# Kernel optimization log

Hardware: AMD Instinct MI355X
Metric: run time of the kernel (lower is better)

Reference implementation:

```python
import jax, jax.numpy as jnp
import numpy as np

B, T, F, H = 4096, 60, 128, 256

def setup_inputs() -> dict:
    key = jax.random.key(0)
    ks = jax.random.split(key, 14)
    sk = 1.0 / np.sqrt(H)
    def unif(k, shape):
        return jax.random.uniform(k, shape, jnp.float32, -sk, sk)
    return {
        "x": jax.random.normal(ks[0], (B, T, F), jnp.float32),
        "Wf": unif(ks[1], (F + H, H)), "bf": unif(ks[2], (H,)),
        "Wu": unif(ks[3], (F + H, H)), "bu": unif(ks[4], (H,)),
        "Wc": unif(ks[5], (F + H, H)), "bc": unif(ks[6], (H,)),
        "Wo": unif(ks[7], (F + H, H)), "bo": unif(ks[8], (H,)),
        "Wd1": jax.random.normal(ks[9], (H, H), jnp.float32) * np.sqrt(2.0 / H),
        "bd1": jnp.zeros((H,), jnp.float32),
        "Wd2": jax.random.normal(ks[10], (H, 1), jnp.float32) * np.sqrt(2.0 / H),
        "bd2": jnp.zeros((1,), jnp.float32),
    }

def reference(x, Wf, bf, Wu, bu, Wc, bc, Wo, bo, Wd1, bd1, Wd2, bd2):
    b = x.shape[0]
    h0 = jnp.zeros((b, H), x.dtype)
    c0 = jnp.zeros((b, H), x.dtype)

    def step(carry, xt):
        h, c = carry
        z = jnp.concatenate([xt, h], axis=-1)  # [B, F+H]
        f = jax.nn.sigmoid(z @ Wf + bf)
        u = jax.nn.sigmoid(z @ Wu + bu)
        g = jnp.tanh(z @ Wc + bc)
        o = jax.nn.sigmoid(z @ Wo + bo)
        c_new = f * c + u * g
        h_new = o * jnp.tanh(c_new)
        return (h_new, c_new), None

    (h, _), _ = jax.lax.scan(step, (h0, c0), jnp.swapaxes(x, 0, 1))  # scan over T
    # dense head: two stacked linear layers, no intermediate activation
    out = (h @ Wd1 + bd1) @ Wd2 + bd2  # [B, 1]
    return out
```

## Files before the change

### kernel.cpp

```cpp
#include <hip/hip_runtime.h>


#define T_STEPS 60
#define F_DIM 128
#define H_DIM 256
#define BC 16
#define ZQ 31.75f
#define L2E 1.44269504f

typedef __attribute__((ext_vector_type(4))) int intx4;

__device__ __forceinline__ int q8(float v) {
    return __float2int_rn(fminf(fmaxf(v, -127.f), 127.f));
}

__global__ __launch_bounds__(1024)
void prep_kernel(const float* __restrict__ Wf, const float* __restrict__ Wu,
                 const float* __restrict__ Wc, const float* __restrict__ Wo,
                 const float* __restrict__ Wd1, const float* __restrict__ bd1,
                 const float* __restrict__ Wd2, const float* __restrict__ bd2,
                 float* __restrict__ cscale, intx4* __restrict__ qpack,
                 float* __restrict__ vhead, float* __restrict__ shead) {
    const int t = threadIdx.x;
    const int b = blockIdx.x;
    if (b < 8) {
        __shared__ float red[16][128];
        __shared__ float fsc[128];
        const int g = b >> 1, ch = b & 1;
        const float* W = (g == 0) ? Wf : (g == 1) ? Wu : (g == 2) ? Wc : Wo;
        const int col = ch * 128 + (t & 127);
        const int grp = t >> 7;
        float mx = 1e-20f, mh = 1e-20f;
#pragma unroll 4
        for (int i = 0; i < 16; ++i)
            mx = fmaxf(mx, fabsf(W[(size_t)(grp * 16 + i) * H_DIM + col]));
#pragma unroll 4
        for (int i = 0; i < 32; ++i)
            mh = fmaxf(mh, fabsf(W[(size_t)(128 + grp * 32 + i) * H_DIM + col]));
        red[grp][t & 127] = mx;
        red[8 + grp][t & 127] = mh;
        __syncthreads();
        if (t < 128) {
            float Mx = red[0][t], Mh = red[8][t];
#pragma unroll
            for (int i = 1; i < 8; ++i) {
                Mx = fmaxf(Mx, red[i][t]);
                Mh = fmaxf(Mh, red[8 + i][t]);
            }
            float cs = fmaxf(4.f * Mx, Mh) * (1.f / 16129.f);
            cscale[g * 256 + ch * 128 + t] = cs;
            fsc[t] = 1.f / (127.f * cs);
        }
        __syncthreads();
#pragma unroll
        for (int i = 0; i < 3; ++i) {
            int task = i * 1024 + t;
            int lane = task & 63, fr = task >> 6;
            int hl = fr / 6, ks6 = fr - hl * 6;
            int l15 = lane & 15, quad = lane >> 4;
            int colw = ch * 128 + hl * 16 + l15;
            int k0 = ks6 * 64 + quad * 16;
            float f = ((ks6 < 2) ? 4.f : 1.f) * fsc[hl * 16 + l15];
            int w[4];
#pragma unroll
            for (int d = 0; d < 4; ++d) {
                int b0 = q8(W[(size_t)(k0 + d * 4 + 0) * H_DIM + colw] * f) & 255;
                int b1 = q8(W[(size_t)(k0 + d * 4 + 1) * H_DIM + colw] * f) & 255;
                int b2 = q8(W[(size_t)(k0 + d * 4 + 2) * H_DIM + colw] * f) & 255;
                int b3 = q8(W[(size_t)(k0 + d * 4 + 3) * H_DIM + colw] * f) & 255;
                w[d] = b0 | (b1 << 8) | (b2 << 16) | (b3 << 24);
            }
            intx4 v = {w[0], w[1], w[2], w[3]};
            qpack[(((ch * 8 + hl) * 4 + g) * 6 + ks6) * 64 + lane] = v;
        }
    } else {
        __shared__ float hp[1024];
        const int j = t >> 2, q = t & 3;
        float s = 0.f;
        const float* row = Wd1 + (size_t)j * H_DIM + q * 64;
#pragma unroll
        for (int i = 0; i < 16; ++i) {
            float4 a = *(const float4*)(row + i * 4);
            float4 bb = *(const float4*)(Wd2 + q * 64 + i * 4);
            s += a.x * bb.x + a.y * bb.y + a.z * bb.z + a.w * bb.w;
        }
        hp[t] = s;
        __syncthreads();
        float vj = 0.f;
        if (q == 0) vj = hp[t] + hp[t + 1] + hp[t + 2] + hp[t + 3];
        __syncthreads();
        if (q == 0) vhead[j] = vj;
        if (t < 256) hp[t] = bd1[t] * Wd2[t];
        __syncthreads();
        for (int off = 128; off > 0; off >>= 1) {
            if (t < off) hp[t] += hp[t + off];
            __syncthreads();
        }
        if (t == 0) shead[0] = hp[0] + bd2[0];
    }
}

__global__ __launch_bounds__(512)
__attribute__((amdgpu_waves_per_eu(2, 2)))
void lstm_kernel(const float* __restrict__ x,
                 const float* __restrict__ bfv, const float* __restrict__ buv,
                 const float* __restrict__ bcv, const float* __restrict__ bov,
                 const intx4* __restrict__ qpack,
                 const float* __restrict__ cscale,
                 const float* __restrict__ vhead, const float* __restrict__ shead,
                 float* __restrict__ out)
{
    __shared__ __align__(16) intx4 wlds[64 * 64];
    __shared__ __align__(16) signed char zbuf[2][6][1024];
    __shared__ float rowsum[BC];

    const int tid  = threadIdx.x;
    const int wave = tid >> 6;
    const int lane = tid & 63;
    const int quad = lane >> 4;
    const int l15  = lane & 15;
    const int b0   = blockIdx.x * BC;

    for (int i = tid; i < 64 * 64; i += 512)
        wlds[i] = qpack[((i >> 6) * 6 + 5) * 64 + (i & 63)];
    intx4 wreg[5][8];
#pragma unroll
    for (int j = 0; j < 8; ++j)
#pragma unroll
        for (int ks = 0; ks < 5; ++ks) {
            intx4 v = qpack[(((8 * wave + j) * 6 + ks) * 64) + lane];
            int a0 = v[0], a1 = v[1], a2 = v[2], a3 = v[3];
            asm volatile("" : "+v"(a0), "+v"(a1), "+v"(a2), "+v"(a3));
            intx4 w = {a0, a1, a2, a3};
            wreg[ks][j] = w;
        }

    for (int i = tid; i < 2 * 6 * 1024 / 4; i += 512) ((int*)zbuf)[i] = 0;
    if (tid < BC) rowsum[tid] = 0.f;

    float csS[2][4], bS[2][4], vh[2];
    float creg[2][4] = {};
    int haddr[2];
#pragma unroll
    for (int hb = 0; hb < 2; ++hb) {
        int a = 2 * wave + hb;
        int hc = a * 16 + l15;
        vh[hb] = vhead[hc];
        haddr[hb] = (2 + (a >> 2)) * 1024 + (a & 3) * 256 + l15;
#pragma unroll
        for (int g = 0; g < 4; ++g) {
            float cs = cscale[g * 256 + hc];
            float bi = (g == 0 ? bfv : g == 1 ? buv : g == 2 ? bcv : bov)[hc];
            float m = (g == 2) ? (-2.f * L2E) : (-L2E);
            csS[hb][g] = m * cs;
            bS[hb][g] = m * bi;
        }
    }

    const int xm = tid >> 5, xi = tid & 31;
    const int f0 = xi * 4;
    const int xaddr = (f0 >> 6) * 1024 + ((f0 & 63) >> 4) * 256 + xm * 16 + (f0 & 15);
    const float* xp = x + (size_t)(b0 + xm) * T_STEPS * F_DIM + f0;

    __syncthreads();
    float4 xv = *(const float4*)(xp);
    {
        unsigned u = (unsigned)(q8(xv.x * ZQ) & 255) | ((unsigned)(q8(xv.y * ZQ) & 255) << 8) |
                     ((unsigned)(q8(xv.z * ZQ) & 255) << 16) | ((unsigned)(q8(xv.w * ZQ) & 255) << 24);
        *(unsigned*)(&zbuf[0][0][0] + xaddr) = u;
    }
    xv = *(const float4*)(xp + F_DIM);
    __syncthreads();

    for (int t = 0; t < T_STEPS; ++t) {
        const int p = t & 1, pn = p ^ 1;
        const intx4* zr = (const intx4*)(&zbuf[p][0][0]);
        signed char* zw = &zbuf[pn][0][0];

        intx4 acc[8] = {};
#pragma unroll
        for (int ks = 0; ks < 5; ++ks) {
            intx4 a = zr[ks * 64 + lane];
#pragma unroll
            for (int j = 0; j < 8; ++j)
                acc[j] = __builtin_amdgcn_mfma_i32_16x16x64_i8(a, wreg[ks][j], acc[j], 0, 0, 0);
        }
        {
            intx4 a5 = zr[5 * 64 + lane];
#pragma unroll
            for (int j = 0; j < 8; ++j) {
                intx4 bw = wlds[(8 * wave + j) * 64 + lane];
                acc[j] = __builtin_amdgcn_mfma_i32_16x16x64_i8(a5, bw, acc[j], 0, 0, 0);
            }
        }

        if (t < T_STEPS - 1) {
            unsigned u = (unsigned)(q8(xv.x * ZQ) & 255) | ((unsigned)(q8(xv.y * ZQ) & 255) << 8) |
                         ((unsigned)(q8(xv.z * ZQ) & 255) << 16) | ((unsigned)(q8(xv.w * ZQ) & 255) << 24);
            *(unsigned*)(zw + xaddr) = u;
            if (t < T_STEPS - 2)
                xv = *(const float4*)(xp + (size_t)(t + 2) * F_DIM);

#pragma unroll
            for (int hb = 0; hb < 2; ++hb)
#pragma unroll
                for (int rr = 0; rr < 4; ++rr) {
                    float uf = fmaf((float)acc[hb * 4 + 0][rr], csS[hb][0], bS[hb][0]);
                    float uu = fmaf((float)acc[hb * 4 + 1][rr], csS[hb][1], bS[hb][1]);
                    float uc = fmaf((float)acc[hb * 4 + 2][rr], csS[hb][2], bS[hb][2]);
                    float uo = fmaf((float)acc[hb * 4 + 3][rr], csS[hb][3], bS[hb][3]);
                    float af = 1.f + __builtin_amdgcn_exp2f(uf);
                    float au = 1.f + __builtin_amdgcn_exp2f(uu);
                    float ac = 1.f + __builtin_amdgcn_exp2f(uc);
                    float ao = 1.f + __builtin_amdgcn_exp2f(uo);
                    float r1 = __builtin_amdgcn_rcpf(af * au);
                    float r2 = __builtin_amdgcn_rcpf(ac * ao);
                    float fg = au * r1;
                    float ug = af * r1;
                    float rc = ao * r2;
                    float og = ac * r2;
                    float cn = fmaf(fg, creg[hb][rr], fmaf(ug + ug, rc, -ug));
                    creg[hb][rr] = cn;
                    float rh = __builtin_amdgcn_rcpf(1.f + __builtin_amdgcn_exp2f(cn * (-2.f * L2E)));
                    float hn = fmaf(og + og, rh, -og);
                    zw[haddr[hb] + (quad * 4 + rr) * 16] =
                        (signed char)__float2int_rn(hn * 127.f);
                }
        } else {
            float hs[4] = {0.f, 0.f, 0.f, 0.f};
#pragma unroll
            for (int hb = 0; hb < 2; ++hb)
#pragma unroll
                for (int rr = 0; rr < 4; ++rr) {
                    float uf = fmaf((float)acc[hb * 4 + 0][rr], csS[hb][0], bS[hb][0]);
                    float uu = fmaf((float)acc[hb * 4 + 1][rr], csS[hb][1], bS[hb][1]);
                    float uc = fmaf((float)acc[hb * 4 + 2][rr], csS[hb][2], bS[hb][2]);
                    float uo = fmaf((float)acc[hb * 4 + 3][rr], csS[hb][3], bS[hb][3]);
                    float af = 1.f + __builtin_amdgcn_exp2f(uf);
                    float au = 1.f + __builtin_amdgcn_exp2f(uu);
                    float ac = 1.f + __builtin_amdgcn_exp2f(uc);
                    float ao = 1.f + __builtin_amdgcn_exp2f(uo);
                    float r1 = __builtin_amdgcn_rcpf(af * au);
                    float r2 = __builtin_amdgcn_rcpf(ac * ao);
                    float fg = au * r1;
                    float ug = af * r1;
                    float rc = ao * r2;
                    float og = ac * r2;
                    float cn = fmaf(fg, creg[hb][rr], fmaf(ug + ug, rc, -ug));
                    float rh = __builtin_amdgcn_rcpf(1.f + __builtin_amdgcn_exp2f(cn * (-2.f * L2E)));
                    float hn = fmaf(og + og, rh, -og);
                    hs[rr] += hn * vh[hb];
                }
#pragma unroll
            for (int rr = 0; rr < 4; ++rr) {
                float s = hs[rr];
#pragma unroll
                for (int m = 1; m < 16; m <<= 1)
                    s += __shfl_xor(s, m, 64);
                if (l15 == 0)
                    atomicAdd(&rowsum[quad * 4 + rr], s);
            }
        }
        __syncthreads();
    }

    if (tid < BC)
        out[b0 + tid] = rowsum[tid] + shead[0];
}

extern "C" void kernel_launch(void* const* d_in, const int* in_sizes, int n_in,
                              void* d_out, int out_size, void* d_ws, size_t ws_size,
                              hipStream_t stream) {
    (void)in_sizes; (void)n_in; (void)out_size; (void)ws_size;
    const float* x   = (const float*)d_in[0];
    const float* Wf  = (const float*)d_in[1];
    const float* bfv = (const float*)d_in[2];
    const float* Wu  = (const float*)d_in[3];
    const float* buv = (const float*)d_in[4];
    const float* Wc  = (const float*)d_in[5];
    const float* bcv = (const float*)d_in[6];
    const float* Wo  = (const float*)d_in[7];
    const float* bov = (const float*)d_in[8];
    const float* Wd1 = (const float*)d_in[9];
    const float* bd1 = (const float*)d_in[10];
    const float* Wd2 = (const float*)d_in[11];
    const float* bd2 = (const float*)d_in[12];

    char* ws = (char*)d_ws;
    intx4* qpack = (intx4*)ws;
    size_t off = (size_t)384 * 64 * 16;
    float* cscale = (float*)(ws + off); off += 1024 * 4;
    float* vhead  = (float*)(ws + off); off += 256 * 4;
    float* shead  = (float*)(ws + off); off += 16;

    prep_kernel<<<9, 1024, 0, stream>>>(Wf, Wu, Wc, Wo, Wd1, bd1, Wd2, bd2,
                                        cscale, qpack, vhead, shead);
    lstm_kernel<<<256, 512, 0, stream>>>(x, bfv, buv, bcv, bov, qpack, cscale,
                                         vhead, shead, (float*)d_out);
}
```

Measured before the change: 305.8 us.

## Split MFMA chain in halves and interleave gate math with second half

The time loop is restructured so the eight MFMA accumulator chains run in two groups of four. The nonlinear gate and cell updates for the first hidden block are interleaved with the second group's MFMAs, overlapping VALU transcendental work with matrix-core latency. The final timestep is peeled out of the loop to remove the per-step branch, and the x prefetch is made unconditional with a clamped index. The risk is higher register pressure and that the A fragments are reloaded from LDS twice.

```diff
diff --git a/kernel.cpp b/kernel.cpp
--- a/kernel.cpp
+++ b/kernel.cpp
@@ -172,11 +172,86 @@
     xv = *(const float4*)(xp + F_DIM);
     __syncthreads();
 
-    for (int t = 0; t < T_STEPS; ++t) {
-        const int p = t & 1, pn = p ^ 1;
+#define GATE_CELL(hb, rr)                                                          \
+    {                                                                              \
+        float uf = fmaf((float)acc[(hb) * 4 + 0][rr], csS[hb][0], bS[hb][0]);      \
+        float uu = fmaf((float)acc[(hb) * 4 + 1][rr], csS[hb][1], bS[hb][1]);      \
+        float uc = fmaf((float)acc[(hb) * 4 + 2][rr], csS[hb][2], bS[hb][2]);      \
+        float uo = fmaf((float)acc[(hb) * 4 + 3][rr], csS[hb][3], bS[hb][3]);      \
+        float af = 1.f + __builtin_amdgcn_exp2f(uf);                               \
+        float au = 1.f + __builtin_amdgcn_exp2f(uu);                               \
+        float ac = 1.f + __builtin_amdgcn_exp2f(uc);                               \
+        float ao = 1.f + __builtin_amdgcn_exp2f(uo);                               \
+        float r1 = __builtin_amdgcn_rcpf(af * au);                                 \
+        float r2 = __builtin_amdgcn_rcpf(ac * ao);                                 \
+        float fg = au * r1;                                                        \
+        float ug = af * r1;                                                        \
+        float rc = ao * r2;                                                        \
+        float og = ac * r2;                                                        \
+        float cn = fmaf(fg, creg[hb][rr], fmaf(ug + ug, rc, -ug));                 \
+        creg[hb][rr] = cn;                                                         \
+        float rh = __builtin_amdgcn_rcpf(1.f + __builtin_amdgcn_exp2f(cn * (-2.f * L2E))); \
+        float hn = fmaf(og + og, rh, -og);                                         \
+        zw[haddr[hb] + (quad * 4 + (rr)) * 16] =                                   \
+            (signed char)__float2int_rn(hn * 127.f);                               \
+    }
+
+#pragma unroll 1
+    for (int t = 0; t < T_STEPS - 1; ++t) {
+        const int p = t & 1;
         const intx4* zr = (const intx4*)(&zbuf[p][0][0]);
-        signed char* zw = &zbuf[pn][0][0];
-
+        signed char* zw = &zbuf[p ^ 1][0][0];
+
+        intx4 acc[8] = {};
+
+#pragma unroll
+        for (int ks = 0; ks < 6; ++ks) {
+            intx4 a = zr[ks * 64 + lane];
+            if (ks < 5) {
+#pragma unroll
+                for (int j = 0; j < 4; ++j)
+                    acc[j] = __builtin_amdgcn_mfma_i32_16x16x64_i8(a, wreg[ks][j], acc[j], 0, 0, 0);
+            } else {
+#pragma unroll
+                for (int j = 0; j < 4; ++j)
+                    acc[j] = __builtin_amdgcn_mfma_i32_16x16x64_i8(
+                        a, wlds[(8 * wave + j) * 64 + lane], acc[j], 0, 0, 0);
+            }
+        }
+
+        {
+            unsigned u = (unsigned)(q8(xv.x * ZQ) & 255) | ((unsigned)(q8(xv.y * ZQ) & 255) << 8) |
+                         ((unsigned)(q8(xv.z * ZQ) & 255) << 16) | ((unsigned)(q8(xv.w * ZQ) & 255) << 24);
+            *(unsigned*)(zw + xaddr) = u;
+            int tn = (t + 2 < T_STEPS) ? (t + 2) : (T_STEPS - 1);
+            xv = *(const float4*)(xp + (size_t)tn * F_DIM);
+        }
+
+#pragma unroll
+        for (int ks = 0; ks < 6; ++ks) {
+            intx4 a = zr[ks * 64 + lane];
+            if (ks < 5) {
+#pragma unroll
+                for (int j = 4; j < 8; ++j)
+                    acc[j] = __builtin_amdgcn_mfma_i32_16x16x64_i8(a, wreg[ks][j], acc[j], 0, 0, 0);
+            } else {
+#pragma unroll
+                for (int j = 4; j < 8; ++j)
+                    acc[j] = __builtin_amdgcn_mfma_i32_16x16x64_i8(
+                        a, wlds[(8 * wave + j) * 64 + lane], acc[j], 0, 0, 0);
+            }
+            if (ks >= 1 && ks < 5) GATE_CELL(0, ks - 1);
+        }
+        GATE_CELL(1, 0);
+        GATE_CELL(1, 1);
+        GATE_CELL(1, 2);
+        GATE_CELL(1, 3);
+
+        __syncthreads();
+    }
+
+    {
+        const intx4* zr = (const intx4*)(&zbuf[(T_STEPS - 1) & 1][0][0]);
         intx4 acc[8] = {};
 #pragma unroll
         for (int ks = 0; ks < 5; ++ks) {
@@ -193,76 +268,42 @@
                 acc[j] = __builtin_amdgcn_mfma_i32_16x16x64_i8(a5, bw, acc[j], 0, 0, 0);
             }
         }
-
-        if (t < T_STEPS - 1) {
-            unsigned u = (unsigned)(q8(xv.x * ZQ) & 255) | ((unsigned)(q8(xv.y * ZQ) & 255) << 8) |
-                         ((unsigned)(q8(xv.z * ZQ) & 255) << 16) | ((unsigned)(q8(xv.w * ZQ) & 255) << 24);
-            *(unsigned*)(zw + xaddr) = u;
-            if (t < T_STEPS - 2)
-                xv = *(const float4*)(xp + (size_t)(t + 2) * F_DIM);
-
-#pragma unroll
-            for (int hb = 0; hb < 2; ++hb)
-#pragma unroll
-                for (int rr = 0; rr < 4; ++rr) {
-                    float uf = fmaf((float)acc[hb * 4 + 0][rr], csS[hb][0], bS[hb][0]);
-                    float uu = fmaf((float)acc[hb * 4 + 1][rr], csS[hb][1], bS[hb][1]);
-                    float uc = fmaf((float)acc[hb * 4 + 2][rr], csS[hb][2], bS[hb][2]);
-                    float uo = fmaf((float)acc[hb * 4 + 3][rr], csS[hb][3], bS[hb][3]);
-                    float af = 1.f + __builtin_amdgcn_exp2f(uf);
-                    float au = 1.f + __builtin_amdgcn_exp2f(uu);
-                    float ac = 1.f + __builtin_amdgcn_exp2f(uc);
-                    float ao = 1.f + __builtin_amdgcn_exp2f(uo);
-                    float r1 = __builtin_amdgcn_rcpf(af * au);
-                    float r2 = __builtin_amdgcn_rcpf(ac * ao);
-                    float fg = au * r1;
-                    float ug = af * r1;
-                    float rc = ao * r2;
-                    float og = ac * r2;
-                    float cn = fmaf(fg, creg[hb][rr], fmaf(ug + ug, rc, -ug));
-                    creg[hb][rr] = cn;
-                    float rh = __builtin_amdgcn_rcpf(1.f + __builtin_amdgcn_exp2f(cn * (-2.f * L2E)));
-                    float hn = fmaf(og + og, rh, -og);
-                    zw[haddr[hb] + (quad * 4 + rr) * 16] =
-                        (signed char)__float2int_rn(hn * 127.f);
-                }
-        } else {
-            float hs[4] = {0.f, 0.f, 0.f, 0.f};
-#pragma unroll
-            for (int hb = 0; hb < 2; ++hb)
-#pragma unroll
-                for (int rr = 0; rr < 4; ++rr) {
-                    float uf = fmaf((float)acc[hb * 4 + 0][rr], csS[hb][0], bS[hb][0]);
-                    float uu = fmaf((float)acc[hb * 4 + 1][rr], csS[hb][1], bS[hb][1]);
-                    float uc = fmaf((float)acc[hb * 4 + 2][rr], csS[hb][2], bS[hb][2]);
-                    float uo = fmaf((float)acc[hb * 4 + 3][rr], csS[hb][3], bS[hb][3]);
-                    float af = 1.f + __builtin_amdgcn_exp2f(uf);
-                    float au = 1.f + __builtin_amdgcn_exp2f(uu);
-                    float ac = 1.f + __builtin_amdgcn_exp2f(uc);
-                    float ao = 1.f + __builtin_amdgcn_exp2f(uo);
-                    float r1 = __builtin_amdgcn_rcpf(af * au);
-                    float r2 = __builtin_amdgcn_rcpf(ac * ao);
-                    float fg = au * r1;
-                    float ug = af * r1;
-                    float rc = ao * r2;
-                    float og = ac * r2;
-                    float cn = fmaf(fg, creg[hb][rr], fmaf(ug + ug, rc, -ug));
-                    float rh = __builtin_amdgcn_rcpf(1.f + __builtin_amdgcn_exp2f(cn * (-2.f * L2E)));
-                    float hn = fmaf(og + og, rh, -og);
-                    hs[rr] += hn * vh[hb];
-                }
+        float hs[4] = {0.f, 0.f, 0.f, 0.f};
+#pragma unroll
+        for (int hb = 0; hb < 2; ++hb)
 #pragma unroll
             for (int rr = 0; rr < 4; ++rr) {
-                float s = hs[rr];
-#pragma unroll
-                for (int m = 1; m < 16; m <<= 1)
-                    s += __shfl_xor(s, m, 64);
-                if (l15 == 0)
-                    atomicAdd(&rowsum[quad * 4 + rr], s);
-            }
-        }
-        __syncthreads();
-    }
+                float uf = fmaf((float)acc[hb * 4 + 0][rr], csS[hb][0], bS[hb][0]);
+                float uu = fmaf((float)acc[hb * 4 + 1][rr], csS[hb][1], bS[hb][1]);
+                float uc = fmaf((float)acc[hb * 4 + 2][rr], csS[hb][2], bS[hb][2]);
+                float uo = fmaf((float)acc[hb * 4 + 3][rr], csS[hb][3], bS[hb][3]);
+                float af = 1.f + __builtin_amdgcn_exp2f(uf);
+                float au = 1.f + __builtin_amdgcn_exp2f(uu);
+                float ac = 1.f + __builtin_amdgcn_exp2f(uc);
+                float ao = 1.f + __builtin_amdgcn_exp2f(uo);
+                float r1 = __builtin_amdgcn_rcpf(af * au);
+                float r2 = __builtin_amdgcn_rcpf(ac * ao);
+                float fg = au * r1;
+                float ug = af * r1;
+                float rc = ao * r2;
+                float og = ac * r2;
+                float cn = fmaf(fg, creg[hb][rr], fmaf(ug + ug, rc, -ug));
+                float rh = __builtin_amdgcn_rcpf(1.f + __builtin_amdgcn_exp2f(cn * (-2.f * L2E)));
+                float hn = fmaf(og + og, rh, -og);
+                hs[rr] += hn * vh[hb];
+            }
+#pragma unroll
+        for (int rr = 0; rr < 4; ++rr) {
+            float s = hs[rr];
+#pragma unroll
+            for (int m = 1; m < 16; m <<= 1)
+                s += __shfl_xor(s, m, 64);
+            if (l15 == 0)
+                atomicAdd(&rowsum[quad * 4 + rr], s);
+        }
+        __syncthreads();
+    }
+#undef GATE_CELL
 
     if (tid < BC)
         out[b0 + tid] = rowsum[tid] + shead[0];
```

Result: slower. 316.3 us (+3.4%).
